# Optimization experiments

Measured on AMD Instinct MI355X. Metric: run time of the kernel, lower is better.

## Reference

```python
import jax, jax.numpy as jnp
import numpy as np

B, T, C, D = 16, 2048, 1024, 128  # batch, seq, n_embd, head_size

def setup_inputs() -> dict:
    key = jax.random.key(0)
    kx, kq, kk, kv = jax.random.split(key, 4)
    x = jax.random.normal(kx, (B, T, C), dtype=jnp.float32)
    s = 1.0 / np.sqrt(C)
    Wq = jax.random.normal(kq, (C, D), dtype=jnp.float32) * s
    Wk = jax.random.normal(kk, (C, D), dtype=jnp.float32) * s
    Wv = jax.random.normal(kv, (C, D), dtype=jnp.float32) * s
    return {"x": x, "Wq": Wq, "Wk": Wk, "Wv": Wv}

def reference(x, Wq, Wk, Wv):
    # q,k,v: [B,T,D]
    q = jnp.einsum('btc,cd->btd', x, Wq)
    k = jnp.einsum('btc,cd->btd', x, Wk)
    v = jnp.einsum('btc,cd->btd', x, Wv)
    scale = 1.0 / jnp.sqrt(jnp.asarray(q.shape[-1], q.dtype))
    wei = jnp.einsum('bqd,bkd->bqk', q, k) * scale  # [B,T,T]
    causal = jnp.tril(jnp.ones((T, T), dtype=bool))
    wei = jnp.where(causal, wei, -jnp.inf)
    wei = jax.nn.softmax(wei, axis=-1)
    # dropout is identity in eval mode
    out = jnp.einsum('bqk,bkd->bqd', wei, v)  # [B,T,D]
    return out
```

## Files before the change

kernel.cpp:

```cpp
#include <hip/hip_runtime.h>

typedef unsigned short u16;
typedef unsigned int   u32;
typedef __attribute__((ext_vector_type(8)))  __bf16 bf16x8;
typedef __attribute__((ext_vector_type(16))) float  f32x16;
typedef __attribute__((ext_vector_type(4)))  float  fl4;
typedef __attribute__((ext_vector_type(4)))  u16    u16x4;
typedef __attribute__((ext_vector_type(4)))  u32    u32x4;

#define NB 16
#define NT 2048
#define NC 1024
#define ND 128


__device__ __forceinline__ u16 f2bf(float f) {
  u32 u = __builtin_bit_cast(u32, f);
  u = (u + 0x7fffu + ((u >> 16) & 1u)) >> 16;
  return (u16)u;
}

__device__ __forceinline__ u32 pk2(float lo, float hi) {
  return (u32)f2bf(lo) | ((u32)f2bf(hi) << 16);
}

__global__ __launch_bounds__(256) void wprep_k(
    const float* __restrict__ Wq, const float* __restrict__ Wk,
    const float* __restrict__ Wv, u16* __restrict__ wf)
{
  const int cb   = blockIdx.x;
  const int kind = cb >> 2;
  const float* __restrict__ W = (kind == 0) ? Wq : (kind == 1) ? Wk : Wv;
  const int lane = threadIdx.x & 63;
  const int ksq  = threadIdx.x >> 6;
  const int l31 = lane & 31, hi = lane >> 5;
  const int d = (cb & 3) * 32 + l31;
  u16* __restrict__ o = wf + (size_t)cb * 64 * 512;
  #pragma unroll 4
  for (int ii = 0; ii < 16; ++ii) {
    int ks = ksq * 16 + ii;
    int k  = ks * 16 + hi * 8;
    u16x4 p0, p1;
    #pragma unroll
    for (int j = 0; j < 4; ++j) p0[j] = f2bf(W[(size_t)(k + j) * ND + d]);
    #pragma unroll
    for (int j = 0; j < 4; ++j) p1[j] = f2bf(W[(size_t)(k + 4 + j) * ND + d]);
    u16* dst = o + ((size_t)ks * 64 + lane) * 8;
    *(u16x4*)dst = p0;
    *(u16x4*)(dst + 4) = p1;
  }
}

__global__ __launch_bounds__(256, 3) void qkv_proj_k(
    const float* __restrict__ x, const u16* __restrict__ wf,
    u16* __restrict__ qf, u16* __restrict__ kf, u16* __restrict__ vf)
{
  const int L    = blockIdx.x;
  const int rt   = L & 255;
  const int kind = L >> 8;
  const int tid  = threadIdx.x;
  const int lane = tid & 63;
  const int wid  = tid >> 6;
  const int wr = wid >> 1, wc = wid & 1;
  const int l31 = lane & 31, hi = lane >> 5;
  const int m0 = rt * 128;

  __shared__ u16 As[128 * 64];

  const int srow = tid >> 4;
  const int sc4  = (tid & 15) * 4;
  const float* __restrict__ xr = x + (size_t)(m0 + srow) * NC + sc4;

  fl4 pA[8];
  auto issueA = [&](int k0) {
    #pragma unroll
    for (int it = 0; it < 8; ++it)
      pA[it] = *(const fl4*)(xr + (size_t)it * 16 * NC + k0);
  };
  auto writeA = [&]() {
    char* b = (char*)As;
    #pragma unroll
    for (int it = 0; it < 8; ++it) {
      int row = it * 16 + srow;
      u16x4 pk;
      pk[0] = __builtin_bit_cast(u16, (__bf16)pA[it][0]);
      pk[1] = __builtin_bit_cast(u16, (__bf16)pA[it][1]);
      pk[2] = __builtin_bit_cast(u16, (__bf16)pA[it][2]);
      pk[3] = __builtin_bit_cast(u16, (__bf16)pA[it][3]);
      *(u16x4*)(b + row * 128 + ((sc4 * 2) ^ ((row & 7) << 4))) = pk;
    }
  };

  const u16* __restrict__ wfb = wf + ((size_t)(kind * 4 + wc * 2) * 64) * 512 + lane * 8;

  f32x16 acc[2][2] = {};

  issueA(0);
  for (int k = 0; k < 16; ++k) {
    writeA();
    if (k < 15) issueA((k + 1) * 64);
    __syncthreads();

    bf16x8 bfr[2][4];
    #pragma unroll
    for (int cb = 0; cb < 2; ++cb)
      #pragma unroll
      for (int ks = 0; ks < 4; ++ks)
        bfr[cb][ks] = *(const bf16x8*)(wfb + ((size_t)cb * 64 + k * 4 + ks) * 512);

    const char* ab = (const char*)As;
    #pragma unroll
    for (int ks = 0; ks < 4; ++ks) {
      #pragma unroll
      for (int fm = 0; fm < 2; ++fm) {
        int row = wr * 64 + fm * 32 + l31;
        bf16x8 a = *(const bf16x8*)(ab + row * 128 + ((ks * 32 + hi * 16) ^ ((row & 7) << 4)));
        #pragma unroll
        for (int cb = 0; cb < 2; ++cb)
          acc[fm][cb] = __builtin_amdgcn_mfma_f32_32x32x16_bf16(a, bfr[cb][ks], acc[fm][cb], 0, 0, 0);
      }
    }
    __syncthreads();
  }

  #pragma unroll
  for (int fm = 0; fm < 2; ++fm) {
    const int t32 = rt * 4 + wr * 2 + fm;
    #pragma unroll
    for (int cb = 0; cb < 2; ++cb) {
      const int d = wc * 64 + cb * 32 + l31;
      if (kind < 2) {
        u16* __restrict__ o = kind ? kf : qf;
        const float sc = kind ? 1.0f : 0.12752539240377073f;
        const int ds = d >> 4, b3 = (d >> 3) & 1, j = d & 7;
        u16* __restrict__ base = o + ((size_t)t32 * 8 + ds) * 512 + 32 * b3 * 8 + j;
        #pragma unroll
        for (int r = 0; r < 16; ++r) {
          int crow = (r & 3) + 8 * (r >> 2) + 4 * hi;
          base[crow * 8] = f2bf(acc[fm][cb][r] * sc);
        }
      } else {
        const int dt = d >> 5;
        #pragma unroll
        for (int g = 0; g < 4; ++g) {
          int c16   = t32 * 2 + (g >> 1);
          int lanep = l31 + 32 * (g & 1);
          u16x4 pk;
          #pragma unroll
          for (int jj = 0; jj < 4; ++jj) pk[jj] = f2bf(acc[fm][cb][g * 4 + jj]);
          *(u16x4*)(vf + (((size_t)c16 * 4 + dt) * 64 + lanep) * 8 + 4 * hi) = pk;
        }
      }
    }
  }
}

__global__ __launch_bounds__(128, 2) void attn_fwd_k(
    const u16* __restrict__ qw, const u16* __restrict__ kw,
    const u16* __restrict__ vw, float* __restrict__ out)
{
  const int tid  = threadIdx.x;
  const int lane = tid & 63;
  const int w    = tid >> 6;
  const int l31  = lane & 31;
  const int hi   = lane >> 5;

  const int c  = blockIdx.x;
  const int bb = (c >> 6) & 15;
  const int qi = ((c & 63) + ((c >> 8) << 4)) & 63;
  const int q0 = qi * 32;
  const int qrow = q0 + l31;

  const u16* __restrict__ qb = qw + ((size_t)bb * 64 + qi) * 4096;
  const u16* __restrict__ kb = kw + (size_t)bb * 64 * 4096;
  const u16* __restrict__ vb = vw + (size_t)bb * 128 * 2048;

  __shared__ float ofs[64][64];
  __shared__ float mls[2][64];

  bf16x8 qfr[8];
  #pragma unroll
  for (int s = 0; s < 8; ++s)
    qfr[s] = *(const bf16x8*)(qb + ((size_t)s * 64 + lane) * 8);

  f32x16 of[4] = {};
  float m_run = -__builtin_inff();
  float l_run = 0.f;

  const int nsteps = (qi >> 1) + 1;
  for (int s = w; s < nsteps; s += 2) {
    const int kv0 = s * 64;
    const bool masked = (s == nsteps - 1);

    bf16x8 kf0[8], kf1[8];
    #pragma unroll
    for (int t = 0; t < 8; ++t) {
      kf0[t] = *(const bf16x8*)(kb + (((size_t)(2 * s) * 8 + t) * 64 + lane) * 8);
      kf1[t] = *(const bf16x8*)(kb + (((size_t)(2 * s + 1) * 8 + t) * 64 + lane) * 8);
    }
    f32x16 st0 = {}, st1 = {};
    #pragma unroll
    for (int t = 0; t < 8; ++t) {
      st0 = __builtin_amdgcn_mfma_f32_32x32x16_bf16(kf0[t], qfr[t], st0, 0, 0, 0);
      st1 = __builtin_amdgcn_mfma_f32_32x32x16_bf16(kf1[t], qfr[t], st1, 0, 0, 0);
    }
    bf16x8 vfr[4][4];
    #pragma unroll
    for (int ks = 0; ks < 4; ++ks)
      #pragma unroll
      for (int dt = 0; dt < 4; ++dt)
        vfr[dt][ks] = *(const bf16x8*)(vb + (((size_t)((kv0 >> 4) + ks) * 4 + dt) * 64 + lane) * 8);

    if (masked) {
      #pragma unroll
      for (int r = 0; r < 16; ++r) {
        int crow = (r & 3) + 8 * (r >> 2) + 4 * hi;
        st0[r] = (kv0 + crow      <= qrow) ? st0[r] : -1e30f;
        st1[r] = (kv0 + 32 + crow <= qrow) ? st1[r] : -1e30f;
      }
    }

    float pmax = -1e30f;
    #pragma unroll
    for (int r = 0; r < 16; ++r) pmax = fmaxf(pmax, fmaxf(st0[r], st1[r]));
    pmax = fmaxf(pmax, __shfl_xor(pmax, 32, 64));

    const bool no_rescale = (pmax <= m_run);
    const float m_new = fmaxf(m_run, pmax);
    const float fac = __builtin_amdgcn_exp2f(m_run - m_new);
    float rsum = 0.f;
    #pragma unroll
    for (int r = 0; r < 16; ++r) {
      st0[r] = __builtin_amdgcn_exp2f(st0[r] - m_new);
      st1[r] = __builtin_amdgcn_exp2f(st1[r] - m_new);
      rsum += st0[r] + st1[r];
    }
    rsum += __shfl_xor(rsum, 32, 64);
    l_run = l_run * fac + rsum;
    m_run = m_new;

    if (!__all(no_rescale)) {
      #pragma unroll
      for (int r = 0; r < 16; ++r) {
        float fr = __shfl(fac, (r & 3) + 8 * (r >> 2) + 4 * hi, 64);
        #pragma unroll
        for (int dt = 0; dt < 4; ++dt) of[dt][r] *= fr;
      }
    }

    u32x4 pa[4];
    #pragma unroll
    for (int g = 0; g < 4; ++g) {
      const float* sp = (g < 2) ? (const float*)&st0 : (const float*)&st1;
      const int o8 = (g & 1) * 8;
      u32 a0 = pk2(sp[o8 + 0], sp[o8 + 1]);
      u32 a1 = pk2(sp[o8 + 2], sp[o8 + 3]);
      u32 b0 = pk2(sp[o8 + 4], sp[o8 + 5]);
      u32 b1 = pk2(sp[o8 + 6], sp[o8 + 7]);
      u32 ta0 = __shfl_xor(a0, 32, 64);
      u32 ta1 = __shfl_xor(a1, 32, 64);
      u32 tb0 = __shfl_xor(b0, 32, 64);
      u32 tb1 = __shfl_xor(b1, 32, 64);
      pa[g][0] = hi ? tb0 : a0;
      pa[g][1] = hi ? tb1 : a1;
      pa[g][2] = hi ? b0  : ta0;
      pa[g][3] = hi ? b1  : ta1;
    }

    #pragma unroll
    for (int ks = 0; ks < 4; ++ks) {
      bf16x8 paf = __builtin_bit_cast(bf16x8, pa[ks]);
      #pragma unroll
      for (int dt = 0; dt < 4; ++dt)
        of[dt] = __builtin_amdgcn_mfma_f32_32x32x16_bf16(paf, vfr[dt][ks], of[dt], 0, 0, 0);
    }
  }

  if (w == 1) {
    #pragma unroll
    for (int dt = 0; dt < 4; ++dt)
      #pragma unroll
      for (int r = 0; r < 16; ++r)
        ofs[dt * 16 + r][lane] = of[dt][r];
    mls[0][lane] = m_run;
    mls[1][lane] = l_run;
  }
  __syncthreads();
  if (w == 0) {
    const float m1 = mls[0][l31];
    const float l1 = mls[1][l31];
    const float mt = fmaxf(m_run, m1);
    const float f0 = __builtin_amdgcn_exp2f(m_run - mt);
    const float f1 = __builtin_amdgcn_exp2f(m1 - mt);
    const float lt = l_run * f0 + l1 * f1;
    const float rl = 1.0f / lt;
    #pragma unroll
    for (int r = 0; r < 16; ++r) {
      int crow = (r & 3) + 8 * (r >> 2) + 4 * hi;
      float f0r = __shfl(f0, crow, 64);
      float f1r = __shfl(f1, crow, 64);
      float lr  = __shfl(rl, crow, 64);
      #pragma unroll
      for (int dt = 0; dt < 4; ++dt)
        out[((size_t)(bb * NT + q0 + crow)) * ND + dt * 32 + l31] =
            (of[dt][r] * f0r + ofs[dt * 16 + r][lane] * f1r) * lr;
    }
  }
}

extern "C" void kernel_launch(void* const* d_in, const int* in_sizes, int n_in,
                              void* d_out, int out_size, void* d_ws, size_t ws_size,
                              hipStream_t stream) {
  (void)in_sizes; (void)n_in; (void)out_size; (void)ws_size;
  const float* x  = (const float*)d_in[0];
  const float* Wq = (const float*)d_in[1];
  const float* Wk = (const float*)d_in[2];
  const float* Wv = (const float*)d_in[3];
  float* out = (float*)d_out;

  u16* qws = (u16*)d_ws;
  u16* kws = qws + (size_t)NB * NT * ND;
  u16* vws = kws + (size_t)NB * NT * ND;
  u16* wfs = vws + (size_t)NB * NT * ND;

  wprep_k<<<dim3(12), dim3(256), 0, stream>>>(Wq, Wk, Wv, wfs);
  qkv_proj_k<<<dim3(768), dim3(256), 0, stream>>>(x, wfs, qws, kws, vws);
  attn_fwd_k<<<dim3(1024), dim3(128), 0, stream>>>(qws, kws, vws, out);
}
```

Measured before the change: 109.2 us.

## Fuse QKV projection tiles to reuse x across Q/K/V and stage weights in LDS

The projection kernel previously had each block compute one of Q, K or V for 128 rows, so x was read three times from global memory. Now each block covers 64 rows and half of the 384 fused output columns (192), so x is read only twice. Weight fragments are staged into LDS with direct global-to-LDS loads instead of per-wave register loads. Occupancy is raised to 4 blocks per SM, and the fp32-to-bf16 conversion moves to the software rounding helper. In exchange there are extra barriers per k-step and a different wave tiling.

```diff
diff --git a/kernel.cpp b/kernel.cpp
--- a/kernel.cpp
+++ b/kernel.cpp
@@ -22,6 +22,12 @@
 
 __device__ __forceinline__ u32 pk2(float lo, float hi) {
   return (u32)f2bf(lo) | ((u32)f2bf(hi) << 16);
+}
+
+__device__ __forceinline__ void gll16(const u16* g, u16* l) {
+  __builtin_amdgcn_global_load_lds(
+      (const __attribute__((address_space(1))) void*)g,
+      (__attribute__((address_space(3))) void*)l, 16, 0, 0);
 }
 
 __global__ __launch_bounds__(256) void wprep_k(
@@ -51,105 +57,99 @@
   }
 }
 
-__global__ __launch_bounds__(256, 3) void qkv_proj_k(
+__global__ __launch_bounds__(256, 4) void qkv_fused_k(
     const float* __restrict__ x, const u16* __restrict__ wf,
     u16* __restrict__ qf, u16* __restrict__ kf, u16* __restrict__ vf)
 {
-  const int L    = blockIdx.x;
-  const int rt   = L & 255;
-  const int kind = L >> 8;
-  const int tid  = threadIdx.x;
+  const int blk = blockIdx.x;
+  const int rt  = blk >> 1;
+  const int h   = blk & 1;
+  const int tid = threadIdx.x;
   const int lane = tid & 63;
   const int wid  = tid >> 6;
-  const int wr = wid >> 1, wc = wid & 1;
+  const int rw = wid & 1, cw = wid >> 1;
   const int l31 = lane & 31, hi = lane >> 5;
-  const int m0 = rt * 128;
-
-  __shared__ u16 As[128 * 64];
-
-  const int srow = tid >> 4;
-  const int sc4  = (tid & 15) * 4;
-  const float* __restrict__ xr = x + (size_t)(m0 + srow) * NC + sc4;
-
-  fl4 pA[8];
+
+  __shared__ u16 As[64 * 64];
+  __shared__ u16 Bs[24 * 512];
+
+  const int arow = tid >> 4;
+  const int ac4  = (tid & 15) * 4;
+  const float* __restrict__ xr = x + ((size_t)rt * 64 + arow) * NC + ac4;
+
+  fl4 pA[4];
   auto issueA = [&](int k0) {
     #pragma unroll
-    for (int it = 0; it < 8; ++it)
-      pA[it] = *(const fl4*)(xr + (size_t)it * 16 * NC + k0);
+    for (int i = 0; i < 4; ++i)
+      pA[i] = *(const fl4*)(xr + (size_t)i * 16 * NC + k0);
   };
   auto writeA = [&]() {
     char* b = (char*)As;
     #pragma unroll
-    for (int it = 0; it < 8; ++it) {
-      int row = it * 16 + srow;
+    for (int i = 0; i < 4; ++i) {
+      int row = i * 16 + arow;
       u16x4 pk;
-      pk[0] = __builtin_bit_cast(u16, (__bf16)pA[it][0]);
-      pk[1] = __builtin_bit_cast(u16, (__bf16)pA[it][1]);
-      pk[2] = __builtin_bit_cast(u16, (__bf16)pA[it][2]);
-      pk[3] = __builtin_bit_cast(u16, (__bf16)pA[it][3]);
-      *(u16x4*)(b + row * 128 + ((sc4 * 2) ^ ((row & 7) << 4))) = pk;
+      pk[0] = f2bf(pA[i][0]); pk[1] = f2bf(pA[i][1]);
+      pk[2] = f2bf(pA[i][2]); pk[3] = f2bf(pA[i][3]);
+      *(u16x4*)(b + row * 128 + ((ac4 * 2) ^ ((row & 7) << 4))) = pk;
     }
   };
 
-  const u16* __restrict__ wfb = wf + ((size_t)(kind * 4 + wc * 2) * 64) * 512 + lane * 8;
-
-  f32x16 acc[2][2] = {};
+  const u16* __restrict__ wfb = wf + (size_t)(h * 6) * 64 * 512;
+
+  f32x16 acc[3] = {};
 
   issueA(0);
   for (int k = 0; k < 16; ++k) {
+    __syncthreads();
     writeA();
+    #pragma unroll
+    for (int j = 0; j < 6; ++j) {
+      int c = wid * 6 + j;
+      gll16(wfb + (((size_t)(c >> 2) * 64 + k * 4 + (c & 3)) * 64 + lane) * 8,
+            &Bs[c * 512]);
+    }
+    __syncthreads();
     if (k < 15) issueA((k + 1) * 64);
-    __syncthreads();
-
-    bf16x8 bfr[2][4];
-    #pragma unroll
-    for (int cb = 0; cb < 2; ++cb)
-      #pragma unroll
-      for (int ks = 0; ks < 4; ++ks)
-        bfr[cb][ks] = *(const bf16x8*)(wfb + ((size_t)cb * 64 + k * 4 + ks) * 512);
-
     const char* ab = (const char*)As;
     #pragma unroll
     for (int ks = 0; ks < 4; ++ks) {
-      #pragma unroll
-      for (int fm = 0; fm < 2; ++fm) {
-        int row = wr * 64 + fm * 32 + l31;
-        bf16x8 a = *(const bf16x8*)(ab + row * 128 + ((ks * 32 + hi * 16) ^ ((row & 7) << 4)));
+      int row = rw * 32 + l31;
+      bf16x8 a = *(const bf16x8*)(ab + row * 128 + ((ks * 32 + hi * 16) ^ ((row & 7) << 4)));
+      #pragma unroll
+      for (int cb = 0; cb < 3; ++cb) {
+        bf16x8 b = *(const bf16x8*)&Bs[((cw * 3 + cb) * 4 + ks) * 512 + lane * 8];
+        acc[cb] = __builtin_amdgcn_mfma_f32_32x32x16_bf16(a, b, acc[cb], 0, 0, 0);
+      }
+    }
+  }
+
+  const int t32 = rt * 2 + rw;
+  #pragma unroll
+  for (int cb = 0; cb < 3; ++cb) {
+    const int colb = h * 192 + cw * 96 + cb * 32;
+    const int kind = colb >> 7;
+    const int d    = (colb & 127) + l31;
+    if (kind < 2) {
+      u16* __restrict__ o = kind ? kf : qf;
+      const float sc = kind ? 1.0f : 0.12752539240377073f;
+      const int ds = d >> 4, b3 = (d >> 3) & 1, j = d & 7;
+      u16* __restrict__ base = o + ((size_t)t32 * 8 + ds) * 512 + 32 * b3 * 8 + j;
+      #pragma unroll
+      for (int r = 0; r < 16; ++r) {
+        int crow = (r & 3) + 8 * (r >> 2) + 4 * hi;
+        base[crow * 8] = f2bf(acc[cb][r] * sc);
+      }
+    } else {
+      const int dt = (d & 127) >> 5;
+      #pragma unroll
+      for (int g = 0; g < 4; ++g) {
+        int c16   = t32 * 2 + (g >> 1);
+        int lanep = l31 + 32 * (g & 1);
+        u16x4 pk;
         #pragma unroll
-        for (int cb = 0; cb < 2; ++cb)
-          acc[fm][cb] = __builtin_amdgcn_mfma_f32_32x32x16_bf16(a, bfr[cb][ks], acc[fm][cb], 0, 0, 0);
-      }
-    }
-    __syncthreads();
-  }
-
-  #pragma unroll
-  for (int fm = 0; fm < 2; ++fm) {
-    const int t32 = rt * 4 + wr * 2 + fm;
-    #pragma unroll
-    for (int cb = 0; cb < 2; ++cb) {
-      const int d = wc * 64 + cb * 32 + l31;
-      if (kind < 2) {
-        u16* __restrict__ o = kind ? kf : qf;
-        const float sc = kind ? 1.0f : 0.12752539240377073f;
-        const int ds = d >> 4, b3 = (d >> 3) & 1, j = d & 7;
-        u16* __restrict__ base = o + ((size_t)t32 * 8 + ds) * 512 + 32 * b3 * 8 + j;
-        #pragma unroll
-        for (int r = 0; r < 16; ++r) {
-          int crow = (r & 3) + 8 * (r >> 2) + 4 * hi;
-          base[crow * 8] = f2bf(acc[fm][cb][r] * sc);
-        }
-      } else {
-        const int dt = d >> 5;
-        #pragma unroll
-        for (int g = 0; g < 4; ++g) {
-          int c16   = t32 * 2 + (g >> 1);
-          int lanep = l31 + 32 * (g & 1);
-          u16x4 pk;
-          #pragma unroll
-          for (int jj = 0; jj < 4; ++jj) pk[jj] = f2bf(acc[fm][cb][g * 4 + jj]);
-          *(u16x4*)(vf + (((size_t)c16 * 4 + dt) * 64 + lanep) * 8 + 4 * hi) = pk;
-        }
+        for (int jj = 0; jj < 4; ++jj) pk[jj] = f2bf(acc[cb][g * 4 + jj]);
+        *(u16x4*)(vf + (((size_t)c16 * 4 + dt) * 64 + lanep) * 8 + 4 * hi) = pk;
       }
     }
   }
@@ -324,6 +324,6 @@
   u16* wfs = vws + (size_t)NB * NT * ND;
 
   wprep_k<<<dim3(12), dim3(256), 0, stream>>>(Wq, Wk, Wv, wfs);
-  qkv_proj_k<<<dim3(768), dim3(256), 0, stream>>>(x, wfs, qws, kws, vws);
+  qkv_fused_k<<<dim3(1024), dim3(256), 0, stream>>>(x, wfs, qws, kws, vws);
   attn_fwd_k<<<dim3(1024), dim3(128), 0, stream>>>(qws, kws, vws, out);
 }
```

Result: faster. 103.8 us (-4.9%).
